# Kernel tuning notes

Hardware: AMD Instinct MI355X
Metric: run time of the kernel (lower is better)

The kernel has to match this reference:

```python
import jax, jax.numpy as jnp
import numpy as np

N = 100000
E = 1600000
F_IN = 64
HEADS = 4
HID = 16
NUM_CLASSES = 2
NEG_SLOPE = 0.2


def setup_inputs() -> dict:
    key = jax.random.key(0)
    ks = jax.random.split(key, 12)
    inputs = jax.random.normal(ks[0], (N, F_IN), dtype=jnp.float32)
    edge_index = jax.random.randint(ks[1], (2, E), 0, N, dtype=jnp.int64)
    edge_attr = jax.random.uniform(ks[2], (E,), dtype=jnp.float32)
    # layer 1 params (GATConv: lin has no bias; final bias of size heads*out)
    s1 = 1.0 / np.sqrt(F_IN)
    W1 = jax.random.uniform(ks[3], (F_IN, HEADS * HID), jnp.float32, -s1, s1)
    att_src1 = jax.random.uniform(ks[4], (HEADS, HID), jnp.float32, -s1, s1)
    att_dst1 = jax.random.uniform(ks[5], (HEADS, HID), jnp.float32, -s1, s1)
    b1 = jnp.zeros((HEADS * HID,), jnp.float32)
    # layer 2 params (heads=1)
    s2 = 1.0 / np.sqrt(HEADS * HID)
    W2 = jax.random.uniform(ks[6], (HEADS * HID, NUM_CLASSES), jnp.float32, -s2, s2)
    att_src2 = jax.random.uniform(ks[7], (1, NUM_CLASSES), jnp.float32, -s2, s2)
    att_dst2 = jax.random.uniform(ks[8], (1, NUM_CLASSES), jnp.float32, -s2, s2)
    b2 = jnp.zeros((NUM_CLASSES,), jnp.float32)
    return {"inputs": inputs, "edge_index": edge_index, "edge_attr": edge_attr,
            "W1": W1, "att_src1": att_src1, "att_dst1": att_dst1, "b1": b1,
            "W2": W2, "att_src2": att_src2, "att_dst2": att_dst2, "b2": b2}


def _add_self_loops(edge_index):
    loop = jnp.arange(N, dtype=edge_index.dtype)
    src = jnp.concatenate([edge_index[0], loop])
    dst = jnp.concatenate([edge_index[1], loop])
    return src, dst


def _gat_layer(x, src, dst, W, a_src, a_dst, bias, heads, out_ch):
    h = (x @ W).reshape(N, heads, out_ch)              # [N,H,C]
    alpha_s = jnp.einsum('nhc,hc->nh', h, a_src)        # [N,H]
    alpha_d = jnp.einsum('nhc,hc->nh', h, a_dst)        # [N,H]
    e = jax.nn.leaky_relu(alpha_s[src] + alpha_d[dst], NEG_SLOPE)  # [E,H]
    # softmax over incoming edges per destination node
    m = jax.ops.segment_max(e, dst, num_segments=N)
    m = jnp.where(jnp.isfinite(m), m, 0.0)
    ex = jnp.exp(e - m[dst])
    denom = jax.ops.segment_sum(ex, dst, num_segments=N)
    alpha = ex / (denom[dst] + 1e-16)                   # [E,H]
    msg = h[src] * alpha[:, :, None]                    # [E,H,C]
    out = jax.ops.segment_sum(msg, dst, num_segments=N) # [N,H,C]
    return out.reshape(N, heads * out_ch) + bias


def reference(inputs, edge_index, edge_attr,
              W1, att_src1, att_dst1, b1,
              W2, att_src2, att_dst2, b2):
    # edge_attr is ignored by GATConv when edge_dim is None (as in the source)
    src, dst = _add_self_loops(edge_index)
    x = _gat_layer(inputs, src, dst, W1, att_src1, att_dst1, b1, HEADS, HID)
    x = jax.nn.relu(x)
    x = _gat_layer(x, src, dst, W2, att_src2, att_dst2, b2, 1, NUM_CLASSES)
    return x
```

## Files before the change

kernel.cpp:

```cpp
#include <hip/hip_runtime.h>
#include <hip/hip_fp16.h>

#define N_NODES 100000
#define NE      1600000
#define ETOT    (NE + N_NODES)
#define F1      64
#define NEG     0.2f
#define CAP     48

#define PBITS   9
#define PSZ     (1 << PBITS)
#define NPART   ((N_NODES + PSZ - 1) / PSZ)
#define N_PAD   (NPART * PSZ)
#define PCAP    10240
#define K2_EPT  8
#define K2_BLK  1024
#define K2_TILE (K2_BLK * K2_EPT)

#define GT      128

static inline int cdiv(int a, int b) { return (a + b - 1) / b; }

__global__ __launch_bounds__(K2_BLK) void partition(
        const int* __restrict__ src, const int* __restrict__ dst,
        int* __restrict__ pcur, int* __restrict__ pairs) {
    __shared__ int hist[NPART];
    __shared__ int base[NPART];
    int t = threadIdx.x;
    for (int i = t; i < NPART; i += K2_BLK) hist[i] = 0;
    __syncthreads();

    int e0 = blockIdx.x * K2_TILE + t;
    int b8[K2_EPT], pos8[K2_EPT], pk8[K2_EPT];
#pragma unroll
    for (int i = 0; i < K2_EPT; ++i) {
        int e = e0 + i * K2_BLK;
        b8[i] = -1;
        if (e < ETOT) {
            int s, d;
            if (e < NE) { s = src[e]; d = dst[e]; } else { s = d = e - NE; }
            int b = d >> PBITS;
            b8[i] = b;
            pk8[i] = ((d & (PSZ - 1)) << 17) | s;
            pos8[i] = atomicAdd(&hist[b], 1);
        }
    }
    __syncthreads();
    for (int i = t; i < NPART; i += K2_BLK)
        base[i] = atomicAdd(&pcur[i], hist[i]);
    __syncthreads();
#pragma unroll
    for (int i = 0; i < K2_EPT; ++i) {
        if (b8[i] >= 0) {
            int idx = base[b8[i]] + pos8[i];
            if (idx < PCAP) pairs[b8[i] * PCAP + idx] = pk8[i];
        }
    }
}

__global__ __launch_bounds__(512) void fine_scatter(
        const int* __restrict__ pcur, const int* __restrict__ pairs,
        int* __restrict__ cnt, int* __restrict__ esrc) {
    __shared__ int lcnt[PSZ];
    __shared__ int lsrc[PSZ * CAP];
    int p = blockIdx.x, t = threadIdx.x;
    for (int i = t; i < PSZ; i += 512) lcnt[i] = 0;
    __syncthreads();

    int np = pcur[p];
    np = np < PCAP ? np : PCAP;
    const int* pp = pairs + p * PCAP;
    for (int i = t; i < np; i += 512) {
        int v = pp[i];
        int ld = v >> 17;
        int s = v & 0x1FFFF;
        int pos = atomicAdd(&lcnt[ld], 1);
        if (pos < CAP) lsrc[ld * CAP + pos] = s;
    }
    __syncthreads();

    int nb = p << PBITS;
    if (t < PSZ && nb + t < N_NODES) cnt[nb + t] = lcnt[t];
    int* eo = esrc + (size_t)nb * CAP;
    for (int i = t; i < PSZ * CAP; i += 512) eo[i] = lsrc[i];
}

__global__ __launch_bounds__(256) void gemm_fused(
        const float* __restrict__ x, const float* __restrict__ W,
        const float* __restrict__ a_src, const float* __restrict__ a_dst,
        __half* __restrict__ h1h, float* __restrict__ as1, float* __restrict__ ad1) {
    __shared__ float sW[64 * 64];
    __shared__ float sXT[64 * 128];
    int t = threadIdx.x;
    int n0 = blockIdx.x * GT;

    for (int i = t; i < 1024; i += 256) ((float4*)sW)[i] = ((const float4*)W)[i];

    for (int i = t; i < 2048; i += 256) {
        int n = i >> 4, kq = i & 15;
        float4 v = make_float4(0.f, 0.f, 0.f, 0.f);
        if (n0 + n < N_NODES) v = ((const float4*)(x + (size_t)(n0 + n) * 64))[kq];
        int k0 = kq * 4, n4 = n >> 2, nl = n & 3;
        sXT[(k0 + 0) * 128 + (((n4 ^ (k0 + 0)) & 31) << 2) + nl] = v.x;
        sXT[(k0 + 1) * 128 + (((n4 ^ (k0 + 1)) & 31) << 2) + nl] = v.y;
        sXT[(k0 + 2) * 128 + (((n4 ^ (k0 + 2)) & 31) << 2) + nl] = v.z;
        sXT[(k0 + 3) * 128 + (((n4 ^ (k0 + 3)) & 31) << 2) + nl] = v.w;
    }
    __syncthreads();

    int jo = t & 7, nq = t >> 3;
    int jo8 = jo * 8;
    float acc[4][8];
#pragma unroll
    for (int m = 0; m < 4; ++m)
#pragma unroll
        for (int c = 0; c < 8; ++c) acc[m][c] = 0.f;

#pragma unroll 4
    for (int k = 0; k < 64; ++k) {
        const float4 xv = *(const float4*)&sXT[k * 128 + (((nq ^ k) & 31) << 2)];
        const float4 w0 = *(const float4*)&sW[k * 64 + jo8];
        const float4 w1 = *(const float4*)&sW[k * 64 + jo8 + 4];
        float xm[4] = {xv.x, xv.y, xv.z, xv.w};
        float wv[8] = {w0.x, w0.y, w0.z, w0.w, w1.x, w1.y, w1.z, w1.w};
#pragma unroll
        for (int m = 0; m < 4; ++m)
#pragma unroll
            for (int c = 0; c < 8; ++c)
                acc[m][c] = fmaf(xm[m], wv[c], acc[m][c]);
    }

    float av[8], dv[8];
#pragma unroll
    for (int c = 0; c < 8; ++c) { av[c] = a_src[jo8 + c]; dv[c] = a_dst[jo8 + c]; }

#pragma unroll
    for (int m = 0; m < 4; ++m) {
        int n = n0 + nq * 4 + m;
        if (n < N_NODES) {
            __half hb[8];
#pragma unroll
            for (int c = 0; c < 8; ++c) hb[c] = __float2half(acc[m][c]);
            *(uint4*)(h1h + (size_t)n * 64 + jo8) = *(const uint4*)hb;
        }
        float ps = 0.f, pd = 0.f;
#pragma unroll
        for (int c = 0; c < 8; ++c) {
            ps = fmaf(acc[m][c], av[c], ps);
            pd = fmaf(acc[m][c], dv[c], pd);
        }
        ps += __shfl_xor(ps, 1, 64);
        pd += __shfl_xor(pd, 1, 64);
        if ((jo & 1) == 0 && n < N_NODES) {
            as1[n * 4 + (jo >> 1)] = ps;
            ad1[n * 4 + (jo >> 1)] = pd;
        }
    }
}

template <int NIT>
__device__ __forceinline__ void rounds(const int* __restrict__ bucket, int deg,
                                       int grp, int sub, int h, float ad,
                                       const __half* __restrict__ h1h,
                                       const float* __restrict__ as1,
                                       float num[8], float& den) {
    int s[NIT];
#pragma unroll
    for (int r = 0; r < NIT; ++r) {
        int ei = r * 8 + grp;
        s[r] = bucket[ei < deg ? ei : 0];
    }
    float a[NIT];
    uint4 g[NIT];
#pragma unroll
    for (int r = 0; r < NIT; ++r) {
        a[r] = as1[s[r] * 4 + h];
        g[r] = *(const uint4*)(h1h + (size_t)s[r] * 64 + sub * 8);
    }
#pragma unroll
    for (int r = 0; r < NIT; ++r) {
        bool act = (r * 8 + grp) < deg;
        float v = a[r] + ad;
        v = v > 0.f ? v : NEG * v;
        float ex = act ? __expf(v) : 0.f;
        const __half2* hp = (const __half2*)&g[r];
#pragma unroll
        for (int q = 0; q < 4; ++q) {
            float2 f = __half22float2(hp[q]);
            num[q * 2 + 0] = fmaf(ex, f.x, num[q * 2 + 0]);
            num[q * 2 + 1] = fmaf(ex, f.y, num[q * 2 + 1]);
        }
        den += ex;
    }
}

__global__ void aggr1(const int* __restrict__ cnt, const int* __restrict__ esrc,
                      const __half* __restrict__ h1h, const float* __restrict__ as1,
                      const float* __restrict__ ad1, const float* __restrict__ b1,
                      const float* __restrict__ W2, const float* __restrict__ a_src2,
                      const float* __restrict__ a_dst2, float4* __restrict__ pack2) {
    int gid = blockIdx.x * blockDim.x + threadIdx.x;
    int w = gid >> 6;
    if (w >= N_NODES) return;
    int lane = threadIdx.x & 63;
    int grp = lane >> 3, sub = lane & 7, h = sub >> 1;
    int deg = cnt[w];
    deg = deg < CAP ? deg : CAP;
    const int* bucket = esrc + (size_t)w * CAP;
    float ad = ad1[w * 4 + h];
    float num[8];
#pragma unroll
    for (int c = 0; c < 8; ++c) num[c] = 0.f;
    float den = 0.f;

    int nit = (deg + 7) >> 3;
    if (nit == 1)      rounds<1>(bucket, deg, grp, sub, h, ad, h1h, as1, num, den);
    else if (nit == 2) rounds<2>(bucket, deg, grp, sub, h, ad, h1h, as1, num, den);
    else if (nit == 3) rounds<3>(bucket, deg, grp, sub, h, ad, h1h, as1, num, den);
    else               rounds<6>(bucket, deg, grp, sub, h, ad, h1h, as1, num, den);

#pragma unroll
    for (int d = 8; d < 64; d <<= 1) {
#pragma unroll
        for (int c = 0; c < 8; ++c) num[c] += __shfl_xor(num[c], d, 64);
        den += __shfl_xor(den, d, 64);
    }
    if (grp == 0) {
        float inv = 1.f / (den + 1e-16f);
        const float4 ba = ((const float4*)b1)[sub * 2];
        const float4 bb = ((const float4*)b1)[sub * 2 + 1];
        float o[8];
        o[0] = fmaf(num[0], inv, ba.x); o[1] = fmaf(num[1], inv, ba.y);
        o[2] = fmaf(num[2], inv, ba.z); o[3] = fmaf(num[3], inv, ba.w);
        o[4] = fmaf(num[4], inv, bb.x); o[5] = fmaf(num[5], inv, bb.y);
        o[6] = fmaf(num[6], inv, bb.z); o[7] = fmaf(num[7], inv, bb.w);
        const float4* w2p = (const float4*)(W2 + sub * 16);
        float4 w2v0 = w2p[0], w2v1 = w2p[1], w2v2 = w2p[2], w2v3 = w2p[3];
        float wtmp[16] = {w2v0.x, w2v0.y, w2v0.z, w2v0.w,
                          w2v1.x, w2v1.y, w2v1.z, w2v1.w,
                          w2v2.x, w2v2.y, w2v2.z, w2v2.w,
                          w2v3.x, w2v3.y, w2v3.z, w2v3.w};
        float p0 = 0.f, p1 = 0.f;
#pragma unroll
        for (int c = 0; c < 8; ++c) {
            float r = fmaxf(o[c], 0.f);
            p0 = fmaf(r, wtmp[c * 2 + 0], p0);
            p1 = fmaf(r, wtmp[c * 2 + 1], p1);
        }
        p0 += __shfl_xor(p0, 1, 64); p1 += __shfl_xor(p1, 1, 64);
        p0 += __shfl_xor(p0, 2, 64); p1 += __shfl_xor(p1, 2, 64);
        p0 += __shfl_xor(p0, 4, 64); p1 += __shfl_xor(p1, 4, 64);
        if (sub == 0) {
            float4 pk;
            pk.x = p0;
            pk.y = p1;
            pk.z = p0 * a_src2[0] + p1 * a_src2[1];
            pk.w = p0 * a_dst2[0] + p1 * a_dst2[1];
            pack2[w] = pk;
        }
    }
}

__global__ void aggr2(const int* __restrict__ cnt, const int* __restrict__ esrc,
                      const float4* __restrict__ pack2, const float* __restrict__ b2,
                      float* __restrict__ out) {
    int d = blockIdx.x * blockDim.x + threadIdx.x;
    if (d >= N_NODES) return;
    int deg = cnt[d];
    deg = deg < CAP ? deg : CAP;
    const int* bucket = esrc + (size_t)d * CAP;
    float adv = pack2[d].w;
    float n0 = 0.f, n1 = 0.f, den = 0.f;
    int i = 0;
    for (; i + 2 <= deg; i += 2) {
        float4 pa = pack2[bucket[i]];
        float4 pb = pack2[bucket[i + 1]];
        float va = pa.z + adv; va = va > 0.f ? va : NEG * va;
        float vb = pb.z + adv; vb = vb > 0.f ? vb : NEG * vb;
        float ea = __expf(va), eb = __expf(vb);
        n0 = fmaf(ea, pa.x, n0); n1 = fmaf(ea, pa.y, n1);
        n0 = fmaf(eb, pb.x, n0); n1 = fmaf(eb, pb.y, n1);
        den += ea + eb;
    }
    if (i < deg) {
        float4 pa = pack2[bucket[i]];
        float va = pa.z + adv; va = va > 0.f ? va : NEG * va;
        float ea = __expf(va);
        n0 = fmaf(ea, pa.x, n0); n1 = fmaf(ea, pa.y, n1);
        den += ea;
    }
    float inv = 1.f / (den + 1e-16f);
    out[d * 2 + 0] = fmaf(n0, inv, b2[0]);
    out[d * 2 + 1] = fmaf(n1, inv, b2[1]);
}

extern "C" void kernel_launch(void* const* d_in, const int* in_sizes, int n_in,
                              void* d_out, int out_size, void* d_ws, size_t ws_size,
                              hipStream_t stream) {
    const float* x        = (const float*)d_in[0];
    const int*   ei       = (const int*)d_in[1];
    const float* W1       = (const float*)d_in[3];
    const float* att_src1 = (const float*)d_in[4];
    const float* att_dst1 = (const float*)d_in[5];
    const float* b1       = (const float*)d_in[6];
    const float* W2       = (const float*)d_in[7];
    const float* att_src2 = (const float*)d_in[8];
    const float* att_dst2 = (const float*)d_in[9];
    const float* b2       = (const float*)d_in[10];

    const int* src = ei;
    const int* dst = ei + NE;
    float* out = (float*)d_out;

    char* p = (char*)d_ws;
    int* pcur     = (int*)p;     p += sizeof(int) * 256;
    int* cnt      = (int*)p;     p += sizeof(int) * N_NODES;
    int* esrc     = (int*)p;     p += sizeof(int) * (size_t)N_PAD * CAP;
    __half* h1h   = (__half*)p;  p += sizeof(__half) * (size_t)N_NODES * F1;
    float* as1    = (float*)p;   p += sizeof(float) * N_NODES * 4;
    float* ad1    = (float*)p;   p += sizeof(float) * N_NODES * 4;
    float4* pack2 = (float4*)p;  p += sizeof(float4) * N_NODES;
    int* pairs    = (int*)p;     p += sizeof(int) * (size_t)NPART * PCAP;

    const int B = 256;

    hipMemsetAsync(pcur, 0, sizeof(int) * 256, stream);
    partition<<<cdiv(ETOT, K2_TILE), K2_BLK, 0, stream>>>(src, dst, pcur, pairs);
    fine_scatter<<<NPART, 512, 0, stream>>>(pcur, pairs, cnt, esrc);

    gemm_fused<<<cdiv(N_NODES, GT), 256, 0, stream>>>(x, W1, att_src1, att_dst1,
                                                      h1h, as1, ad1);

    aggr1<<<cdiv(N_NODES * 64, B), B, 0, stream>>>(cnt, esrc, h1h, as1, ad1, b1,
                                                   W2, att_src2, att_dst2, pack2);

    aggr2<<<cdiv(N_NODES, B), B, 0, stream>>>(cnt, esrc, pack2, b2, out);
}
```

Baseline: 203.3 us.

## Fuse fine scatter with GEMM, shrink partitions, wave-per-node layer-2 aggregation

Merges the fine scatter and the layer-1 GEMM into one launch, with blocks split by index and a shared-memory union, so the two independent stages overlap and one launch is removed. Partition size is halved, with smaller blocks for partitioning, to fit the new 256-thread block and raise parallelism. Layer-2 aggregation now assigns one wavefront per node, with one edge per lane and a shuffle reduction, instead of a serial per-thread loop. This launches many more threads. Halving PCAP leaves less slack against partition overflow.

```diff
diff --git a/kernel.cpp b/kernel.cpp
--- a/kernel.cpp
+++ b/kernel.cpp
@@ -8,16 +8,17 @@
 #define NEG     0.2f
 #define CAP     48
 
-#define PBITS   9
+#define PBITS   8
 #define PSZ     (1 << PBITS)
 #define NPART   ((N_NODES + PSZ - 1) / PSZ)
 #define N_PAD   (NPART * PSZ)
-#define PCAP    10240
+#define PCAP    5120
 #define K2_EPT  8
-#define K2_BLK  1024
+#define K2_BLK  256
 #define K2_TILE (K2_BLK * K2_EPT)
 
 #define GT      128
+#define GEMM_NBLK ((N_NODES + GT - 1) / GT)
 
 static inline int cdiv(int a, int b) { return (a + b - 1) / b; }
 
@@ -58,53 +59,57 @@
     }
 }
 
-__global__ __launch_bounds__(512) void fine_scatter(
+__global__ __launch_bounds__(256) void fs_gemm(
         const int* __restrict__ pcur, const int* __restrict__ pairs,
-        int* __restrict__ cnt, int* __restrict__ esrc) {
-    __shared__ int lcnt[PSZ];
-    __shared__ int lsrc[PSZ * CAP];
-    int p = blockIdx.x, t = threadIdx.x;
-    for (int i = t; i < PSZ; i += 512) lcnt[i] = 0;
-    __syncthreads();
-
-    int np = pcur[p];
-    np = np < PCAP ? np : PCAP;
-    const int* pp = pairs + p * PCAP;
-    for (int i = t; i < np; i += 512) {
-        int v = pp[i];
-        int ld = v >> 17;
-        int s = v & 0x1FFFF;
-        int pos = atomicAdd(&lcnt[ld], 1);
-        if (pos < CAP) lsrc[ld * CAP + pos] = s;
-    }
-    __syncthreads();
-
-    int nb = p << PBITS;
-    if (t < PSZ && nb + t < N_NODES) cnt[nb + t] = lcnt[t];
-    int* eo = esrc + (size_t)nb * CAP;
-    for (int i = t; i < PSZ * CAP; i += 512) eo[i] = lsrc[i];
-}
-
-__global__ __launch_bounds__(256) void gemm_fused(
+        int* __restrict__ cnt, int* __restrict__ esrc,
         const float* __restrict__ x, const float* __restrict__ W,
         const float* __restrict__ a_src, const float* __restrict__ a_dst,
         __half* __restrict__ h1h, float* __restrict__ as1, float* __restrict__ ad1) {
-    __shared__ float sW[64 * 64];
-    __shared__ float sXT[64 * 128];
+    __shared__ union {
+        struct { float sW[64 * 64]; float sXT[64 * 128]; } g;
+        struct { int lcnt[PSZ]; int lsrc[PSZ * CAP]; } f;
+    } u;
     int t = threadIdx.x;
-    int n0 = blockIdx.x * GT;
-
-    for (int i = t; i < 1024; i += 256) ((float4*)sW)[i] = ((const float4*)W)[i];
+
+    if (blockIdx.x < NPART) {
+        int p = blockIdx.x;
+        for (int i = t; i < PSZ; i += 256) u.f.lcnt[i] = 0;
+        __syncthreads();
+
+        int np = pcur[p];
+        np = np < PCAP ? np : PCAP;
+        const int* pp = pairs + p * PCAP;
+        for (int i = t; i < np; i += 256) {
+            int v = pp[i];
+            int ld = v >> 17;
+            int s = v & 0x1FFFF;
+            int pos = atomicAdd(&u.f.lcnt[ld], 1);
+            if (pos < CAP) u.f.lsrc[ld * CAP + pos] = s;
+        }
+        __syncthreads();
+
+        int nb = p << PBITS;
+        for (int i = t; i < PSZ; i += 256)
+            if (nb + i < N_NODES) cnt[nb + i] = u.f.lcnt[i];
+        int* eo = esrc + (size_t)nb * CAP;
+        for (int i = t; i < PSZ * CAP; i += 256) eo[i] = u.f.lsrc[i];
+        return;
+    }
+
+    int n0 = (blockIdx.x - NPART) * GT;
+
+    for (int i = t; i < 1024; i += 256)
+        ((float4*)u.g.sW)[i] = ((const float4*)W)[i];
 
     for (int i = t; i < 2048; i += 256) {
         int n = i >> 4, kq = i & 15;
         float4 v = make_float4(0.f, 0.f, 0.f, 0.f);
         if (n0 + n < N_NODES) v = ((const float4*)(x + (size_t)(n0 + n) * 64))[kq];
         int k0 = kq * 4, n4 = n >> 2, nl = n & 3;
-        sXT[(k0 + 0) * 128 + (((n4 ^ (k0 + 0)) & 31) << 2) + nl] = v.x;
-        sXT[(k0 + 1) * 128 + (((n4 ^ (k0 + 1)) & 31) << 2) + nl] = v.y;
-        sXT[(k0 + 2) * 128 + (((n4 ^ (k0 + 2)) & 31) << 2) + nl] = v.z;
-        sXT[(k0 + 3) * 128 + (((n4 ^ (k0 + 3)) & 31) << 2) + nl] = v.w;
+        u.g.sXT[(k0 + 0) * 128 + (((n4 ^ (k0 + 0)) & 31) << 2) + nl] = v.x;
+        u.g.sXT[(k0 + 1) * 128 + (((n4 ^ (k0 + 1)) & 31) << 2) + nl] = v.y;
+        u.g.sXT[(k0 + 2) * 128 + (((n4 ^ (k0 + 2)) & 31) << 2) + nl] = v.z;
+        u.g.sXT[(k0 + 3) * 128 + (((n4 ^ (k0 + 3)) & 31) << 2) + nl] = v.w;
     }
     __syncthreads();
 
@@ -118,9 +123,9 @@
 
 #pragma unroll 4
     for (int k = 0; k < 64; ++k) {
-        const float4 xv = *(const float4*)&sXT[k * 128 + (((nq ^ k) & 31) << 2)];
-        const float4 w0 = *(const float4*)&sW[k * 64 + jo8];
-        const float4 w1 = *(const float4*)&sW[k * 64 + jo8 + 4];
+        const float4 xv = *(const float4*)&u.g.sXT[k * 128 + (((nq ^ k) & 31) << 2)];
+        const float4 w0 = *(const float4*)&u.g.sW[k * 64 + jo8];
+        const float4 w1 = *(const float4*)&u.g.sW[k * 64 + jo8 + 4];
         float xm[4] = {xv.x, xv.y, xv.z, xv.w};
         float wv[8] = {w0.x, w0.y, w0.z, w0.w, w1.x, w1.y, w1.z, w1.w};
 #pragma unroll
@@ -181,7 +186,7 @@
     for (int r = 0; r < NIT; ++r) {
         bool act = (r * 8 + grp) < deg;
         float v = a[r] + ad;
-        v = v > 0.f ? v : NEG * v;
+        v = fmaxf(v, NEG * v);
         float ex = act ? __expf(v) : 0.f;
         const __half2* hp = (const __half2*)&g[r];
 #pragma unroll
@@ -264,34 +269,34 @@
 __global__ void aggr2(const int* __restrict__ cnt, const int* __restrict__ esrc,
                       const float4* __restrict__ pack2, const float* __restrict__ b2,
                       float* __restrict__ out) {
-    int d = blockIdx.x * blockDim.x + threadIdx.x;
-    if (d >= N_NODES) return;
-    int deg = cnt[d];
+    int gid = blockIdx.x * blockDim.x + threadIdx.x;
+    int w = gid >> 6;
+    if (w >= N_NODES) return;
+    int lane = threadIdx.x & 63;
+    int deg = cnt[w];
     deg = deg < CAP ? deg : CAP;
-    const int* bucket = esrc + (size_t)d * CAP;
-    float adv = pack2[d].w;
-    float n0 = 0.f, n1 = 0.f, den = 0.f;
-    int i = 0;
-    for (; i + 2 <= deg; i += 2) {
-        float4 pa = pack2[bucket[i]];
-        float4 pb = pack2[bucket[i + 1]];
-        float va = pa.z + adv; va = va > 0.f ? va : NEG * va;
-        float vb = pb.z + adv; vb = vb > 0.f ? vb : NEG * vb;
-        float ea = __expf(va), eb = __expf(vb);
-        n0 = fmaf(ea, pa.x, n0); n1 = fmaf(ea, pa.y, n1);
-        n0 = fmaf(eb, pb.x, n0); n1 = fmaf(eb, pb.y, n1);
-        den += ea + eb;
-    }
-    if (i < deg) {
-        float4 pa = pack2[bucket[i]];
-        float va = pa.z + adv; va = va > 0.f ? va : NEG * va;
-        float ea = __expf(va);
-        n0 = fmaf(ea, pa.x, n0); n1 = fmaf(ea, pa.y, n1);
-        den += ea;
-    }
-    float inv = 1.f / (den + 1e-16f);
-    out[d * 2 + 0] = fmaf(n0, inv, b2[0]);
-    out[d * 2 + 1] = fmaf(n1, inv, b2[1]);
+    const int* bucket = esrc + (size_t)w * CAP;
+    float adv = pack2[w].w;
+    bool act = lane < deg;
+    int s = bucket[act ? lane : 0];
+    float4 ps = pack2[s];
+    float v = ps.z + adv;
+    v = fmaxf(v, NEG * v);
+    float ex = act ? __expf(v) : 0.f;
+    float n0 = ex * ps.x, n1 = ex * ps.y, den = ex;
+#pragma unroll
+    for (int d = 1; d < 64; d <<= 1) {
+        n0  += __shfl_xor(n0, d, 64);
+        n1  += __shfl_xor(n1, d, 64);
+        den += __shfl_xor(den, d, 64);
+    }
+    if (lane == 0) {
+        float inv = 1.f / (den + 1e-16f);
+        float2 o;
+        o.x = fmaf(n0, inv, b2[0]);
+        o.y = fmaf(n1, inv, b2[1]);
+        *(float2*)(out + w * 2) = o;
+    }
 }
 
 extern "C" void kernel_launch(void* const* d_in, const int* in_sizes, int n_in,
@@ -313,7 +318,7 @@
     float* out = (float*)d_out;
 
     char* p = (char*)d_ws;
-    int* pcur     = (int*)p;     p += sizeof(int) * 256;
+    int* pcur     = (int*)p;     p += sizeof(int) * 512;
     int* cnt      = (int*)p;     p += sizeof(int) * N_NODES;
     int* esrc     = (int*)p;     p += sizeof(int) * (size_t)N_PAD * CAP;
     __half* h1h   = (__half*)p;  p += sizeof(__half) * (size_t)N_NODES * F1;
@@ -324,15 +329,12 @@
 
     const int B = 256;
 
-    hipMemsetAsync(pcur, 0, sizeof(int) * 256, stream);
+    hipMemsetAsync(pcur, 0, sizeof(int) * 512, stream);
     partition<<<cdiv(ETOT, K2_TILE), K2_BLK, 0, stream>>>(src, dst, pcur, pairs);
-    fine_scatter<<<NPART, 512, 0, stream>>>(pcur, pairs, cnt, esrc);
-
-    gemm_fused<<<cdiv(N_NODES, GT), 256, 0, stream>>>(x, W1, att_src1, att_dst1,
-                                                      h1h, as1, ad1);
-
+    fs_gemm<<<NPART + GEMM_NBLK, 256, 0, stream>>>(pcur, pairs, cnt, esrc,
+                                                   x, W1, att_src1, att_dst1,
+                                                   h1h, as1, ad1);
     aggr1<<<cdiv(N_NODES * 64, B), B, 0, stream>>>(cnt, esrc, h1h, as1, ad1, b1,
                                                    W2, att_src2, att_dst2, pack2);
-
-    aggr2<<<cdiv(N_NODES, B), B, 0, stream>>>(cnt, esrc, pack2, b2, out);
-}
+    aggr2<<<cdiv(N_NODES * 64, B), B, 0, stream>>>(cnt, esrc, pack2, b2, out);
+}
```

New measurement: 220.2 us. 8.3% more time.
